# Kernel tuning notes

Measured on AMD Instinct MI355X. Metric: run time of the kernel, lower is better.

## Reference

```python
import jax, jax.numpy as jnp
import numpy as np

DIM, HEADS = 128, 8
DH = DIM // HEADS
SCALE = DH ** -0.5
N, E = 50000, 800000


def setup_inputs() -> dict:
    key = jax.random.key(0)
    ks = jax.random.split(key, 12)
    w = lambda k: jax.random.normal(k, (DIM, DIM), dtype=jnp.float32) * 0.02
    b = lambda k: jax.random.normal(k, (DIM,), dtype=jnp.float32) * 0.02
    return {
        "q_nodes": jax.random.normal(ks[0], (N, DIM), dtype=jnp.float32),
        "k_edges": jax.random.normal(ks[1], (E, DIM), dtype=jnp.float32),
        "v_edges": jax.random.normal(ks[2], (E, DIM), dtype=jnp.float32),
        "edge_index": jax.random.randint(ks[3], (2, E), 0, N, dtype=jnp.int64),
        "Wq": w(ks[4]), "bq": b(ks[5]),
        "Wk": w(ks[6]), "bk": b(ks[7]),
        "Wv": w(ks[8]), "bv": b(ks[9]),
        "Wo": w(ks[10]), "bo": b(ks[11]),
    }


def reference(q_nodes, k_edges, v_edges, edge_index, Wq, bq, Wk, bk, Wv, bv, Wo, bo):
    n, e = q_nodes.shape[0], k_edges.shape[0]
    dst = edge_index[0]  # src (edge_index[1]) is unused by the module
    q = (q_nodes @ Wq.T + bq).reshape(n, HEADS, DH)
    k = (k_edges @ Wk.T + bk).reshape(e, HEADS, DH)
    v = (v_edges @ Wv.T + bv).reshape(e, HEADS, DH)
    # per-edge score: dot(q[dst], k) per head -> [E, H]
    score = jnp.einsum('ehd,ehd->eh', q[dst], k) * SCALE
    # segment (per-dst-node) softmax over edges, numerically stable
    m = jax.ops.segment_max(score, dst, num_segments=n)          # [N, H]
    ex = jnp.exp(score - m[dst])                                  # [E, H]
    s = jax.ops.segment_sum(ex, dst, num_segments=n)             # [N, H]
    w = ex / (s[dst] + 1e-16)                                     # [E, H]
    weighted_v = (v * w[..., None]).reshape(e, DIM)               # [E, dim]
    aggr = jax.ops.segment_sum(weighted_v, dst, num_segments=n)  # [N, dim]
    return aggr @ Wo.T + bo
```

## Files before the change

### kernel.cpp

```cpp
#include <hip/hip_runtime.h>

#define TM 64
#define NTHREADS 256
#define PAD 132

typedef __attribute__((ext_vector_type(8))) short short8;
typedef __attribute__((ext_vector_type(4))) float f32x4;

__device__ __forceinline__ short f2bf(float f) {
  union { float f; unsigned u; } uf; uf.f = f;
  unsigned r = uf.u + 0x7FFFu + ((uf.u >> 16) & 1u);
  return (short)(r >> 16);
}
__device__ __forceinline__ float bf2f(short s) {
  union { unsigned u; float f; } uf; uf.u = ((unsigned)(unsigned short)s) << 16;
  return uf.f;
}
__device__ __forceinline__ short8 pack8(float4 a, float4 b) {
  short8 r;
  r[0] = f2bf(a.x); r[1] = f2bf(a.y); r[2] = f2bf(a.z); r[3] = f2bf(a.w);
  r[4] = f2bf(b.x); r[5] = f2bf(b.y); r[6] = f2bf(b.z); r[7] = f2bf(b.w);
  return r;
}


__global__ __launch_bounds__(512) void proj_mfma(
    const float* __restrict__ X, const short* __restrict__ Wb,
    const float* __restrict__ bias, float* __restrict__ Y, int M, float scale) {
  __shared__ short Xb[8192];
  int t = threadIdx.x;
  int w = t >> 6, l = t & 63, g = l >> 4, c = l & 15;
  short8 wf[4];
#pragma unroll
  for (int kc = 0; kc < 4; ++kc)
    wf[kc] = *(const short8*)(Wb + (w * 16 + c) * 128 + kc * 32 + g * 8);
  float4 b4 = *(const float4*)(bias + w * 16 + g * 4);

  for (int rb = blockIdx.x * 64; rb < M; rb += gridDim.x * 64) {
    {
      int r = t >> 3, q8 = t & 7;
      int row = rb + r; if (row >= M) row = M - 1;
      const float4* xs = (const float4*)(X + (size_t)row * 128 + q8 * 16);
      float4 x0 = xs[0], x1 = xs[1], x2 = xs[2], x3 = xs[3];
      int sw = (r & 7) << 4;
      *(short8*)((char*)Xb + r * 256 + ((q8 * 32) ^ sw)) = pack8(x0, x1);
      *(short8*)((char*)Xb + r * 256 + ((q8 * 32 + 16) ^ sw)) = pack8(x2, x3);
    }
    __syncthreads();
#pragma unroll
    for (int et = 0; et < 4; ++et) {
      int rl = et * 16 + c;
      f32x4 acc = {};
      int sw = (rl & 7) << 4;
#pragma unroll
      for (int kc = 0; kc < 4; ++kc) {
        short8 xb = *(const short8*)((char*)Xb + rl * 256 + ((kc * 64 + g * 16) ^ sw));
        acc = __builtin_amdgcn_mfma_f32_16x16x32_bf16(wf[kc], xb, acc, 0, 0, 0);
      }
      int row = rb + rl;
      if (row < M) {
        float4 o;
        o.x = (acc[0] + b4.x) * scale; o.y = (acc[1] + b4.y) * scale;
        o.z = (acc[2] + b4.z) * scale; o.w = (acc[3] + b4.w) * scale;
        *(float4*)(Y + (size_t)row * 128 + w * 16 + g * 4) = o;
      }
    }
    __syncthreads();
  }
}


__global__ __launch_bounds__(512) void proj_mfma_h(
    const float* __restrict__ X, const short* __restrict__ Wb,
    const float* __restrict__ bias, short* __restrict__ Yh, int M, float scale) {
  __shared__ short Xb[8192];
  int t = threadIdx.x;
  int w = t >> 6, l = t & 63, g = l >> 4, c = l & 15;
  short8 wf[4];
#pragma unroll
  for (int kc = 0; kc < 4; ++kc)
    wf[kc] = *(const short8*)(Wb + (w * 16 + c) * 128 + kc * 32 + g * 8);
  float4 b4 = *(const float4*)(bias + w * 16 + g * 4);

  for (int rb = blockIdx.x * 64; rb < M; rb += gridDim.x * 64) {
    {
      int r = t >> 3, q8 = t & 7;
      int row = rb + r; if (row >= M) row = M - 1;
      const float4* xs = (const float4*)(X + (size_t)row * 128 + q8 * 16);
      float4 x0 = xs[0], x1 = xs[1], x2 = xs[2], x3 = xs[3];
      int sw = (r & 7) << 4;
      *(short8*)((char*)Xb + r * 256 + ((q8 * 32) ^ sw)) = pack8(x0, x1);
      *(short8*)((char*)Xb + r * 256 + ((q8 * 32 + 16) ^ sw)) = pack8(x2, x3);
    }
    __syncthreads();
#pragma unroll
    for (int et = 0; et < 4; ++et) {
      int rl = et * 16 + c;
      f32x4 acc = {};
      int sw = (rl & 7) << 4;
#pragma unroll
      for (int kc = 0; kc < 4; ++kc) {
        short8 xb = *(const short8*)((char*)Xb + rl * 256 + ((kc * 64 + g * 16) ^ sw));
        acc = __builtin_amdgcn_mfma_f32_16x16x32_bf16(wf[kc], xb, acc, 0, 0, 0);
      }
      int row = rb + rl;
      if (row < M) {
        short4 o;
        o.x = f2bf((acc[0] + b4.x) * scale); o.y = f2bf((acc[1] + b4.y) * scale);
        o.z = f2bf((acc[2] + b4.z) * scale); o.w = f2bf((acc[3] + b4.w) * scale);
        *(short4*)(Yh + (size_t)row * 128 + w * 16 + g * 4) = o;
      }
    }
    __syncthreads();
  }
}


__global__ __launch_bounds__(256) void hist_kernel(const int* __restrict__ dst,
                                                   int* __restrict__ cnt, int E) {
  int e = blockIdx.x * 256 + threadIdx.x;
  if (e < E) atomicAdd(&cnt[dst[e]], 1);
// ... 8 lines not shown
  for (int d = 1; d < 64; d <<= 1) v += __shfl_xor(v, d);
  if ((t & 63) == 0) ws[t >> 6] = v;
  __syncthreads();
  if (t < 16) {
    int x = ws[t];
#pragma unroll
    for (int d = 1; d < 16; d <<= 1) x += __shfl_xor(x, d);
    if (t == 0) part[blockIdx.x] = x;
  }
}

__global__ __launch_bounds__(64) void scan_offs(int* __restrict__ part, int P) {
  int t = threadIdx.x;
  int carry = 0;
  for (int base = 0; base < P; base += 64) {
    int i = base + t;
    int v = (i < P) ? part[i] : 0;
    int x = v;
#pragma unroll
    for (int d = 1; d < 64; d <<= 1) { int y = __shfl_up(x, d); if (t >= d) x += y; }
    if (i < P) part[i] = x - v + carry;
    carry += __shfl(x, 63);
  }
}

__global__ __launch_bounds__(1024) void scan_final(const int* __restrict__ cnt,
                                                   const int* __restrict__ part,
                                                   int* __restrict__ rp,
                                                   int* __restrict__ cur, int N) {
  __shared__ int ws[16];
  __shared__ int wofs[16];
  int t = threadIdx.x, i = blockIdx.x * 1024 + t;
  int lane = t & 63, wid = t >> 6;
  int v = (i < N) ? cnt[i] : 0;
  int x = v;
#pragma unroll
  for (int d = 1; d < 64; d <<= 1) { int y = __shfl_up(x, d); if (lane >= d) x += y; }
  if (lane == 63) ws[wid] = x;
  __syncthreads();
  if (t == 0) {
    int s = 0;
#pragma unroll
    for (int k2 = 0; k2 < 16; ++k2) { int tmp = ws[k2]; wofs[k2] = s; s += tmp; }
  }
  __syncthreads();
  int incl = x + wofs[wid] + part[blockIdx.x];
  int excl = incl - v;
  if (i < N) {
    rp[i] = excl; cur[i] = excl;
    if (i == N - 1) rp[N] = incl;
  }
}

__global__ __launch_bounds__(256) void perm_kernel(const int* __restrict__ dst,
                                                   int* __restrict__ cursor,
                                                   int* __restrict__ perm, int E) {
  int e = blockIdx.x * 256 + threadIdx.x;
  if (e < E) perm[e] = atomicAdd(&cursor[dst[e]], 1);
}

__global__ __launch_bounds__(256) void wprep4(
    const float* __restrict__ Wq, const float* __restrict__ Wk,
    const float* __restrict__ Wv, const float* __restrict__ Wo,
    short* __restrict__ wqb, short* __restrict__ wkb,
    short* __restrict__ wvb, short* __restrict__ wob) {
  int i = blockIdx.x * 256 + threadIdx.x;
  if (i < 16384) {
    wqb[i] = f2bf(Wq[i]); wkb[i] = f2bf(Wk[i]);
    wvb[i] = f2bf(Wv[i]); wob[i] = f2bf(Wo[i]);
  }
}


__global__ __launch_bounds__(512) void edge_mfma7(
    const float* __restrict__ K, const float* __restrict__ V,
    const int* __restrict__ eidx, const int* __restrict__ perm,
    const short* __restrict__ wkb, const short* __restrict__ wvb,
    const float* __restrict__ bk, const short* __restrict__ qpb,
    float* __restrict__ exb, short* __restrict__ wv, int E) {
  __shared__ short Kb[8192];
  __shared__ short Vb[8192];
  __shared__ float exs[512];
  __shared__ int sh_perm[64];
  int t = threadIdx.x;
  int w = t >> 6, l = t & 63, g = l >> 4, c = l & 15;
  float4 bk4 = *(const float4*)(bk + w * 16 + g * 4);
  const short* wkp = wkb + (w * 16 + c) * 128 + g * 8;
  const short* wvp = wvb + (w * 16 + c) * 128 + g * 8;
  const short* qpp = qpb + (size_t)(w * 16 + g * 4);

  int r = t >> 3, q8 = t & 7;
  int sw_st = (r & 7) << 4;
  int b0 = r * 256 + ((q8 * 32) ^ sw_st);
  int stride = gridDim.x * 64;
  int eb = blockIdx.x * 64;

  float4 k0, k1, k2, k3;
  short4 qvb[4];
  int prm_r;
  {
    int row0 = eb + r; if (row0 >= E) row0 = E - 1;
    const float4* ks = (const float4*)(K + (size_t)row0 * 128 + q8 * 16);
    k0 = ks[0]; k1 = ks[1]; k2 = ks[2]; k3 = ks[3];
    prm_r = perm[row0];
#pragma unroll
    for (int et = 0; et < 4; ++et) {
      int e = eb + et * 16 + c; if (e >= E) e = E - 1;
      qvb[et] = *(const short4*)(qpp + (size_t)eidx[e] * 128);
    }
  }

  for (; eb < E; eb += stride) {
    int ebn = eb + stride;
    bool hn = ebn < E;

    __syncthreads();
    *(short8*)((char*)Kb + b0) = pack8(k0, k1);
    *(short8*)((char*)Kb + (b0 ^ 16)) = pack8(k2, k3);
    if (q8 == 0) sh_perm[r] = prm_r;
    short8 wK[4];
#pragma unroll
    for (int kc = 0; kc < 4; ++kc)
      wK[kc] = *(const short8*)(wkp + kc * 32);
    float4 v0, v1, v2, v3;
    {
      int rowv = eb + r; if (rowv >= E) rowv = E - 1;
      const float4* vs = (const float4*)(V + (size_t)rowv * 128 + q8 * 16);
      v0 = vs[0]; v1 = vs[1]; v2 = vs[2]; v3 = vs[3];
    }
    __syncthreads();

    float ex[4];
#pragma unroll
    for (int et = 0; et < 4; ++et) {
      int eloc = et * 16 + c;
      int swr = (eloc & 7) << 4;
      f32x4 acc = {};
#pragma unroll
      for (int kc = 0; kc < 4; ++kc) {
        short8 xb = *(const short8*)((char*)Kb + eloc * 256 + ((kc * 64 + g * 16) ^ swr));
        acc = __builtin_amdgcn_mfma_f32_16x16x32_bf16(wK[kc], xb, acc, 0, 0, 0);
      }
      float s = (acc[0] + bk4.x) * bf2f(qvb[et].x) + (acc[1] + bk4.y) * bf2f(qvb[et].y) +
                (acc[2] + bk4.z) * bf2f(qvb[et].z) + (acc[3] + bk4.w) * bf2f(qvb[et].w);
      s += __shfl_xor(s, 16);
      s += __shfl_xor(s, 32);
      ex[et] = __expf(s);
      if (g == 0) exs[eloc * 8 + w] = ex[et];
    }

    *(short8*)((char*)Vb + b0) = pack8(v0, v1);
    *(short8*)((char*)Vb + (b0 ^ 16)) = pack8(v2, v3);
    short8 wV[4];
#pragma unroll
    for (int kc = 0; kc < 4; ++kc)
      wV[kc] = *(const short8*)(wvp + kc * 32);
    int prm_rn = 0;
    if (hn) {
      int rowk = ebn + r; if (rowk >= E) rowk = E - 1;
      const float4* ks = (const float4*)(K + (size_t)rowk * 128 + q8 * 16);
      k0 = ks[0]; k1 = ks[1]; k2 = ks[2]; k3 = ks[3];
      prm_rn = perm[rowk];
#pragma unroll
      for (int et = 0; et < 4; ++et) {
        int e = ebn + et * 16 + c; if (e >= E) e = E - 1;
        qvb[et] = *(const short4*)(qpp + (size_t)eidx[e] * 128);
      }
    }
    __syncthreads();

#pragma unroll
    for (int et = 0; et < 4; ++et) {
      int eloc = et * 16 + c;
      int swr = (eloc & 7) << 4;
      f32x4 acc = {};
#pragma unroll
      for (int kc = 0; kc < 4; ++kc) {
        short8 xb = *(const short8*)((char*)Vb + eloc * 256 + ((kc * 64 + g * 16) ^ swr));
        acc = __builtin_amdgcn_mfma_f32_16x16x32_bf16(wV[kc], xb, acc, 0, 0, 0);
      }
      short4 sv;
      sv.x = f2bf(acc[0] * ex[et]); sv.y = f2bf(acc[1] * ex[et]);
      sv.z = f2bf(acc[2] * ex[et]); sv.w = f2bf(acc[3] * ex[et]);
      *(short4*)((char*)Kb + eloc * 256 + ((w * 32 + g * 8) ^ swr)) = sv;
    }
    prm_r = prm_rn;
    __syncthreads();

    {
      int row = eb + r;
      if (row < E) {
        int slot = sh_perm[r];
        short8 a = *(const short8*)((char*)Kb + r * 256 + ((q8 * 32) ^ sw_st));
        short8 b = *(const short8*)((char*)Kb + r * 256 + ((q8 * 32 + 16) ^ sw_st));
        *(short8*)(wv + (size_t)slot * 128 + q8 * 16) = a;
        *(short8*)(wv + (size_t)slot * 128 + q8 * 16 + 8) = b;
      }
      if (t < 128) {
        int r2 = t >> 1, half = t & 1;
        if (eb + r2 < E) {
          int slot2 = sh_perm[r2];
          *(float4*)(exb + (size_t)slot2 * 8 + half * 4) =
              *(const float4*)(&exs[r2 * 8 + half * 4]);
        }
      }
    }
  }
}


__global__ __launch_bounds__(256) void pull3(
    const short* __restrict__ wv, const float* __restrict__ exb,
    const int* __restrict__ rp, const float* __restrict__ bv,
    float* __restrict__ aggr, int N) {
  int w = threadIdx.x >> 6, l = threadIdx.x & 63;
  int n = blockIdx.x * 4 + w;
  if (n >= N) return;
  int beg = rp[n], end = rp[n + 1];
  int h = l >> 3;
  float a0 = 0.f, a1 = 0.f, s = 0.f;
  int j = beg;
  for (; j + 1 < end; j += 2) {
    unsigned u0 = *(const unsigned*)(wv + (size_t)j * 128 + l * 2);
    unsigned u1 = *(const unsigned*)(wv + (size_t)(j + 1) * 128 + l * 2);
    float s0 = exb[(size_t)j * 8 + h], s1 = exb[(size_t)(j + 1) * 8 + h];
    a0 += bf2f((short)(u0 & 0xFFFFu)) + bf2f((short)(u1 & 0xFFFFu));
    a1 += bf2f((short)(u0 >> 16)) + bf2f((short)(u1 >> 16));
    s += s0 + s1;
  }
  if (j < end) {
    unsigned u0 = *(const unsigned*)(wv + (size_t)j * 128 + l * 2);
    s += exb[(size_t)j * 8 + h];
    a0 += bf2f((short)(u0 & 0xFFFFu));
    a1 += bf2f((short)(u0 >> 16));
  }
  float2 o;
  if (end > beg) {
    float inv = 1.f / (s + 1e-16f);
    float2 bvv = *(const float2*)(bv + l * 2);
    o.x = a0 * inv + bvv.x; o.y = a1 * inv + bvv.y;
  } else {
    o.x = 0.f; o.y = 0.f;
  }
  *(float2*)(aggr + (size_t)n * 128 + l * 2) = o;
}


__device__ __forceinline__ void stage_x(float (*Xs)[PAD], const float* __restrict__ X,
                                        int rowbase, int M, int t) {
#pragma unroll
  for (int i = 0; i < 8; ++i) {
    int idx = t + NTHREADS * i;
    int r = idx >> 5, q = idx & 31;
    int row = rowbase + r;
    if (row >= M) row = M - 1;
    const float4 v = *(const float4*)(X + (size_t)row * 128 + q * 4);
    *(float4*)(&Xs[r][q * 4]) = v;
  }
}

__device__ __forceinline__ void gemm_tile(const float (*Xs)[PAD], float (*WT)[PAD],
                                          const float* __restrict__ W,
                                          float acc[8][4], int r0, int c0, int t) {
#pragma unroll 1
  for (int kk = 0; kk < 128; kk += 32) {
    {
      int j = t >> 1, half = t & 1;
      const float* src = W + j * 128 + kk + half * 16;
      float4 a = *(const float4*)(src);
      float4 b = *(const float4*)(src + 4);
      float4 c = *(const float4*)(src + 8);
      float4 d = *(const float4*)(src + 12);
      int cb = half * 16;
      WT[cb + 0][j] = a.x;  WT[cb + 1][j] = a.y;  WT[cb + 2][j] = a.z;  WT[cb + 3][j] = a.w;
      WT[cb + 4][j] = b.x;  WT[cb + 5][j] = b.y;  WT[cb + 6][j] = b.z;  WT[cb + 7][j] = b.w;
      WT[cb + 8][j] = c.x;  WT[cb + 9][j] = c.y;  WT[cb + 10][j] = c.z; WT[cb + 11][j] = c.w;
      WT[cb + 12][j] = d.x; WT[cb + 13][j] = d.y; WT[cb + 14][j] = d.z; WT[cb + 15][j] = d.w;
    }
    __syncthreads();
#pragma unroll
    for (int c2 = 0; c2 < 16; ++c2) {
      float4 wa = *(const float4*)(&WT[2 * c2][c0]);
      float4 wb = *(const float4*)(&WT[2 * c2 + 1][c0]);
#pragma unroll
      for (int i = 0; i < 8; ++i) {
        float2 xv = *(const float2*)(&Xs[r0 + i][kk + 2 * c2]);
        acc[i][0] = fmaf(xv.x, wa.x, acc[i][0]);
        acc[i][1] = fmaf(xv.x, wa.y, acc[i][1]);
        acc[i][2] = fmaf(xv.x, wa.z, acc[i][2]);
        acc[i][3] = fmaf(xv.x, wa.w, acc[i][3]);
        acc[i][0] = fmaf(xv.y, wb.x, acc[i][0]);
        acc[i][1] = fmaf(xv.y, wb.y, acc[i][1]);
        acc[i][2] = fmaf(xv.y, wb.z, acc[i][2]);
        acc[i][3] = fmaf(xv.y, wb.w, acc[i][3]);
      }
    }
    __syncthreads();
// ... 95 lines not shown
  int B0 = blockIdx.x * TM;
#pragma unroll
  for (int i = 0; i < 8; ++i) {
    int idx = t + NTHREADS * i;
    int r = idx >> 5, q = idx & 31;
    int row = B0 + r;
    if (row >= M) row = M - 1;
    float4 v = *(const float4*)(aggr + (size_t)row * 128 + q * 4);
    float inv = 1.0f / (s_sum[(size_t)row * 8 + (q >> 2)] + 1e-16f);
    v.x *= inv; v.y *= inv; v.z *= inv; v.w *= inv;
    *(float4*)(&Xs[r][q * 4]) = v;
  }
  __syncthreads();
  int r0 = (t >> 5) * 8, m = t & 31, c0 = m * 4;
  float acc[8][4] = {};
  gemm_tile(Xs, WT, W, acc, r0, c0, t);
  float4 bv = ((const float4*)b)[m];
#pragma unroll
  for (int i = 0; i < 8; ++i) {
    int row = B0 + r0 + i;
    if (row < M) {
      float4 o;
      o.x = acc[i][0] + bv.x; o.y = acc[i][1] + bv.y;
      o.z = acc[i][2] + bv.z; o.w = acc[i][3] + bv.w;
      *(float4*)(Y + (size_t)row * 128 + c0) = o;
    }
  }
}


extern "C" void kernel_launch(void* const* d_in, const int* in_sizes, int n_in,
                              void* d_out, int out_size, void* d_ws, size_t ws_size,
                              hipStream_t stream) {
  const float* q_nodes = (const float*)d_in[0];
  const float* k_edges = (const float*)d_in[1];
  const float* v_edges = (const float*)d_in[2];
  const int* eidx = (const int*)d_in[3];
  const float* Wq = (const float*)d_in[4];
  const float* bq = (const float*)d_in[5];
  const float* Wk = (const float*)d_in[6];
  const float* bk = (const float*)d_in[7];
  const float* Wv = (const float*)d_in[8];
  const float* bv = (const float*)d_in[9];
  const float* Wo = (const float*)d_in[10];
  const float* bo = (const float*)d_in[11];

  int N = in_sizes[0] / 128;
  int E = in_sizes[1] / 128;
  int P = (N + 1023) / 1024;

  size_t off = 0;
  auto alloc = [&](size_t b) { size_t o = off; off += (b + 255) & ~(size_t)255; return o; };
  size_t o_qpb  = alloc((size_t)N * 128 * 2);
  size_t o_aggr = alloc((size_t)N * 128 * 4);
  size_t o_exb  = alloc((size_t)E * 8 * 4);
  size_t o_rp   = alloc(((size_t)N + 1) * 4);
  size_t o_cur  = alloc((size_t)N * 4);
  size_t o_cnt  = alloc((size_t)N * 4);
  size_t o_perm = alloc((size_t)E * 4);
  size_t o_part = alloc((size_t)(P + 1) * 4);
  size_t o_wqb  = alloc((size_t)16384 * 2);
  size_t o_wkb  = alloc((size_t)16384 * 2);
  size_t o_wvb  = alloc((size_t)16384 * 2);
  size_t o_wob  = alloc((size_t)16384 * 2);
  size_t o_wv   = alloc((size_t)E * 128 * 2);

  if (off <= ws_size) {
    char* base = (char*)d_ws;
    short* qpb   = (short*)(base + o_qpb);
    float* aggr  = (float*)(base + o_aggr);
    float* exb   = (float*)(base + o_exb);
    int*   rp    = (int*)(base + o_rp);
    int*   cur   = (int*)(base + o_cur);
    int*   cnt   = (int*)(base + o_cnt);
    int*   perm  = (int*)(base + o_perm);
    int*   part  = (int*)(base + o_part);
    short* wqb   = (short*)(base + o_wqb);
    short* wkb   = (short*)(base + o_wkb);
    short* wvb   = (short*)(base + o_wvb);
    short* wob   = (short*)(base + o_wob);
    short* wvbuf = (short*)(base + o_wv);

    hipMemsetAsync(cnt, 0, (size_t)N * 4, stream);
    wprep4<<<64, 256, 0, stream>>>(Wq, Wk, Wv, Wo, wqb, wkb, wvb, wob);
    proj_mfma_h<<<(N + 63) / 64, 512, 0, stream>>>(q_nodes, wqb, bq, qpb, N, 0.25f);
    hist_kernel<<<(E + 255) / 256, 256, 0, stream>>>(eidx, cnt, E);
    scan_part<<<P, 1024, 0, stream>>>(cnt, part, N);
    scan_offs<<<1, 64, 0, stream>>>(part, P);
    scan_final<<<P, 1024, 0, stream>>>(cnt, part, rp, cur, N);
    perm_kernel<<<(E + 255) / 256, 256, 0, stream>>>(eidx, cur, perm, E);

    int eblk = (E + 63) / 64; if (eblk > 1024) eblk = 1024;
    edge_mfma7<<<eblk, 512, 0, stream>>>(k_edges, v_edges, eidx, perm, wkb, wvb,
                                         bk, qpb, exb, wvbuf, E);
    pull3<<<(N + 3) / 4, 256, 0, stream>>>(wvbuf, exb, rp, bv, aggr, N);
    proj_mfma<<<(N + 63) / 64, 512, 0, stream>>>(aggr, wob, bo, (float*)d_out, N, 1.0f);
  } else {
    float* q_proj = (float*)d_ws;
    float* s_sum  = q_proj + (size_t)N * 128;
    float* aggr   = s_sum + (size_t)N * 8;
    hipMemsetAsync(s_sum, 0, (size_t)N * 136 * sizeof(float), stream);
    int nblk = (N + TM - 1) / TM;
    int eblk = (E + TM - 1) / TM;
    proj_kernel<<<nblk, NTHREADS, 0, stream>>>(q_nodes, Wq, bq, q_proj, N);
    edge_kernel<<<eblk, NTHREADS, 0, stream>>>(k_edges, v_edges, eidx, Wk, bk, Wv, bv,
                                               q_proj, s_sum, aggr, E);
    out_kernel<<<nblk, NTHREADS, 0, stream>>>(aggr, s_sum, Wo, bo, (float*)d_out, N);
  }
}
```

Baseline: 420.0 us.

## Defer V projection until after aggregation via per-head raw-V sums

The V projection moves out of the per-edge kernel and is applied after aggregation, using linearity. Each node gathers raw fp32 V rows by sorted edge id and accumulates eight per-head weighted sums, stored as bf16 [N,8,128]. A fused kernel then applies Wv per head block plus bias, and Wo plus bias, in one pass. This removes the per-edge V MFMA and the E x 128 bf16 weighted-V buffer, at the cost of random fp32 V gathers, an 8x wider per-node intermediate and an extra eid scatter.

```diff
diff --git a/kernel.cpp b/kernel.cpp
--- a/kernel.cpp
+++ b/kernel.cpp
@@ -21,52 +21,6 @@
   r[0] = f2bf(a.x); r[1] = f2bf(a.y); r[2] = f2bf(a.z); r[3] = f2bf(a.w);
   r[4] = f2bf(b.x); r[5] = f2bf(b.y); r[6] = f2bf(b.z); r[7] = f2bf(b.w);
   return r;
-}
-
-
-__global__ __launch_bounds__(512) void proj_mfma(
-    const float* __restrict__ X, const short* __restrict__ Wb,
-    const float* __restrict__ bias, float* __restrict__ Y, int M, float scale) {
-  __shared__ short Xb[8192];
-  int t = threadIdx.x;
-  int w = t >> 6, l = t & 63, g = l >> 4, c = l & 15;
-  short8 wf[4];
-#pragma unroll
-  for (int kc = 0; kc < 4; ++kc)
-    wf[kc] = *(const short8*)(Wb + (w * 16 + c) * 128 + kc * 32 + g * 8);
-  float4 b4 = *(const float4*)(bias + w * 16 + g * 4);
-
-  for (int rb = blockIdx.x * 64; rb < M; rb += gridDim.x * 64) {
-    {
-      int r = t >> 3, q8 = t & 7;
-      int row = rb + r; if (row >= M) row = M - 1;
-      const float4* xs = (const float4*)(X + (size_t)row * 128 + q8 * 16);
-      float4 x0 = xs[0], x1 = xs[1], x2 = xs[2], x3 = xs[3];
-      int sw = (r & 7) << 4;
-      *(short8*)((char*)Xb + r * 256 + ((q8 * 32) ^ sw)) = pack8(x0, x1);
-      *(short8*)((char*)Xb + r * 256 + ((q8 * 32 + 16) ^ sw)) = pack8(x2, x3);
-    }
-    __syncthreads();
-#pragma unroll
-    for (int et = 0; et < 4; ++et) {
-      int rl = et * 16 + c;
-      f32x4 acc = {};
-      int sw = (rl & 7) << 4;
-#pragma unroll
-      for (int kc = 0; kc < 4; ++kc) {
-        short8 xb = *(const short8*)((char*)Xb + rl * 256 + ((kc * 64 + g * 16) ^ sw));
-        acc = __builtin_amdgcn_mfma_f32_16x16x32_bf16(wf[kc], xb, acc, 0, 0, 0);
-      }
-      int row = rb + rl;
-      if (row < M) {
-        float4 o;
-        o.x = (acc[0] + b4.x) * scale; o.y = (acc[1] + b4.y) * scale;
-        o.z = (acc[2] + b4.z) * scale; o.w = (acc[3] + b4.w) * scale;
-        *(float4*)(Y + (size_t)row * 128 + w * 16 + g * 4) = o;
-      }
-    }
-    __syncthreads();
-  }
 }
 
 
@@ -181,11 +135,15 @@
   }
 }
 
-__global__ __launch_bounds__(256) void perm_kernel(const int* __restrict__ dst,
-                                                   int* __restrict__ cursor,
-                                                   int* __restrict__ perm, int E) {
+__global__ __launch_bounds__(256) void perm_eid(const int* __restrict__ dst,
+                                                int* __restrict__ cursor,
+                                                int* __restrict__ perm,
+                                                int* __restrict__ eid, int E) {
   int e = blockIdx.x * 256 + threadIdx.x;
-  if (e < E) perm[e] = atomicAdd(&cursor[dst[e]], 1);
+  if (e < E) {
+    int p = atomicAdd(&cursor[dst[e]], 1);
+    perm[e] = p; eid[p] = e;
+  }
 }
 
 __global__ __launch_bounds__(256) void wprep4(
@@ -201,40 +159,33 @@
 }
 
 
-__global__ __launch_bounds__(512) void edge_mfma7(
-    const float* __restrict__ K, const float* __restrict__ V,
-    const int* __restrict__ eidx, const int* __restrict__ perm,
-    const short* __restrict__ wkb, const short* __restrict__ wvb,
+__global__ __launch_bounds__(512) void kproj_score(
+    const float* __restrict__ K, const int* __restrict__ eidx,
+    const int* __restrict__ perm, const short* __restrict__ wkb,
     const float* __restrict__ bk, const short* __restrict__ qpb,
-    float* __restrict__ exb, short* __restrict__ wv, int E) {
+    float* __restrict__ exb, int E) {
   __shared__ short Kb[8192];
-  __shared__ short Vb[8192];
-  __shared__ float exs[512];
-  __shared__ int sh_perm[64];
   int t = threadIdx.x;
   int w = t >> 6, l = t & 63, g = l >> 4, c = l & 15;
   float4 bk4 = *(const float4*)(bk + w * 16 + g * 4);
   const short* wkp = wkb + (w * 16 + c) * 128 + g * 8;
-  const short* wvp = wvb + (w * 16 + c) * 128 + g * 8;
   const short* qpp = qpb + (size_t)(w * 16 + g * 4);
-
   int r = t >> 3, q8 = t & 7;
-  int sw_st = (r & 7) << 4;
-  int b0 = r * 256 + ((q8 * 32) ^ sw_st);
+  int b0 = r * 256 + ((q8 * 32) ^ ((r & 7) << 4));
   int stride = gridDim.x * 64;
   int eb = blockIdx.x * 64;
 
   float4 k0, k1, k2, k3;
   short4 qvb[4];
-  int prm_r;
+  int p[4];
   {
     int row0 = eb + r; if (row0 >= E) row0 = E - 1;
     const float4* ks = (const float4*)(K + (size_t)row0 * 128 + q8 * 16);
     k0 = ks[0]; k1 = ks[1]; k2 = ks[2]; k3 = ks[3];
-    prm_r = perm[row0];
 #pragma unroll
     for (int et = 0; et < 4; ++et) {
       int e = eb + et * 16 + c; if (e >= E) e = E - 1;
+      p[et] = perm[e];
       qvb[et] = *(const short4*)(qpp + (size_t)eidx[e] * 128);
     }
   }
@@ -242,24 +193,15 @@
   for (; eb < E; eb += stride) {
     int ebn = eb + stride;
     bool hn = ebn < E;
-
     __syncthreads();
     *(short8*)((char*)Kb + b0) = pack8(k0, k1);
     *(short8*)((char*)Kb + (b0 ^ 16)) = pack8(k2, k3);
-    if (q8 == 0) sh_perm[r] = prm_r;
     short8 wK[4];
 #pragma unroll
     for (int kc = 0; kc < 4; ++kc)
       wK[kc] = *(const short8*)(wkp + kc * 32);
-    float4 v0, v1, v2, v3;
-    {
-      int rowv = eb + r; if (rowv >= E) rowv = E - 1;
-      const float4* vs = (const float4*)(V + (size_t)rowv * 128 + q8 * 16);
-      v0 = vs[0]; v1 = vs[1]; v2 = vs[2]; v3 = vs[3];
-    }
-    __syncthreads();
-
-    float ex[4];
+    __syncthreads();
+
 #pragma unroll
     for (int et = 0; et < 4; ++et) {
       int eloc = et * 16 + c;
@@ -274,104 +216,126 @@
                 (acc[2] + bk4.z) * bf2f(qvb[et].z) + (acc[3] + bk4.w) * bf2f(qvb[et].w);
       s += __shfl_xor(s, 16);
       s += __shfl_xor(s, 32);
-      ex[et] = __expf(s);
-      if (g == 0) exs[eloc * 8 + w] = ex[et];
-    }
-
-    *(short8*)((char*)Vb + b0) = pack8(v0, v1);
-    *(short8*)((char*)Vb + (b0 ^ 16)) = pack8(v2, v3);
-    short8 wV[4];
-#pragma unroll
-    for (int kc = 0; kc < 4; ++kc)
-      wV[kc] = *(const short8*)(wvp + kc * 32);
-    int prm_rn = 0;
+      if (g == 0) exb[(size_t)p[et] * 8 + w] = __expf(s);
+    }
+
     if (hn) {
       int rowk = ebn + r; if (rowk >= E) rowk = E - 1;
       const float4* ks = (const float4*)(K + (size_t)rowk * 128 + q8 * 16);
       k0 = ks[0]; k1 = ks[1]; k2 = ks[2]; k3 = ks[3];
-      prm_rn = perm[rowk];
 #pragma unroll
       for (int et = 0; et < 4; ++et) {
         int e = ebn + et * 16 + c; if (e >= E) e = E - 1;
+        p[et] = perm[e];
         qvb[et] = *(const short4*)(qpp + (size_t)eidx[e] * 128);
       }
     }
-    __syncthreads();
-
-#pragma unroll
-    for (int et = 0; et < 4; ++et) {
-      int eloc = et * 16 + c;
-      int swr = (eloc & 7) << 4;
-      f32x4 acc = {};
-#pragma unroll
-      for (int kc = 0; kc < 4; ++kc) {
-        short8 xb = *(const short8*)((char*)Vb + eloc * 256 + ((kc * 64 + g * 16) ^ swr));
-        acc = __builtin_amdgcn_mfma_f32_16x16x32_bf16(wV[kc], xb, acc, 0, 0, 0);
-      }
-      short4 sv;
-      sv.x = f2bf(acc[0] * ex[et]); sv.y = f2bf(acc[1] * ex[et]);
-      sv.z = f2bf(acc[2] * ex[et]); sv.w = f2bf(acc[3] * ex[et]);
-      *(short4*)((char*)Kb + eloc * 256 + ((w * 32 + g * 8) ^ swr)) = sv;
-    }
-    prm_r = prm_rn;
-    __syncthreads();
-
-    {
-      int row = eb + r;
-      if (row < E) {
-        int slot = sh_perm[r];
-        short8 a = *(const short8*)((char*)Kb + r * 256 + ((q8 * 32) ^ sw_st));
-        short8 b = *(const short8*)((char*)Kb + r * 256 + ((q8 * 32 + 16) ^ sw_st));
-        *(short8*)(wv + (size_t)slot * 128 + q8 * 16) = a;
-        *(short8*)(wv + (size_t)slot * 128 + q8 * 16 + 8) = b;
-      }
-      if (t < 128) {
-        int r2 = t >> 1, half = t & 1;
-        if (eb + r2 < E) {
-          int slot2 = sh_perm[r2];
-          *(float4*)(exb + (size_t)slot2 * 8 + half * 4) =
-              *(const float4*)(&exs[r2 * 8 + half * 4]);
-        }
-      }
-    }
-  }
-}
-
-
-__global__ __launch_bounds__(256) void pull3(
-    const short* __restrict__ wv, const float* __restrict__ exb,
-    const int* __restrict__ rp, const float* __restrict__ bv,
-    float* __restrict__ aggr, int N) {
-  int w = threadIdx.x >> 6, l = threadIdx.x & 63;
-  int n = blockIdx.x * 4 + w;
+  }
+}
+
+
+__global__ __launch_bounds__(256) void vpull(
+    const float* __restrict__ V, const int* __restrict__ eid,
+    const int* __restrict__ rp, const float* __restrict__ exb,
+    short* __restrict__ araw, int N) {
+  int wn = threadIdx.x >> 6, l = threadIdx.x & 63;
+  int n = blockIdx.x * 4 + wn;
   if (n >= N) return;
   int beg = rp[n], end = rp[n + 1];
-  int h = l >> 3;
-  float a0 = 0.f, a1 = 0.f, s = 0.f;
-  int j = beg;
-  for (; j + 1 < end; j += 2) {
-    unsigned u0 = *(const unsigned*)(wv + (size_t)j * 128 + l * 2);
-    unsigned u1 = *(const unsigned*)(wv + (size_t)(j + 1) * 128 + l * 2);
-    float s0 = exb[(size_t)j * 8 + h], s1 = exb[(size_t)(j + 1) * 8 + h];
-    a0 += bf2f((short)(u0 & 0xFFFFu)) + bf2f((short)(u1 & 0xFFFFu));
-    a1 += bf2f((short)(u0 >> 16)) + bf2f((short)(u1 >> 16));
-    s += s0 + s1;
-  }
-  if (j < end) {
-    unsigned u0 = *(const unsigned*)(wv + (size_t)j * 128 + l * 2);
-    s += exb[(size_t)j * 8 + h];
-    a0 += bf2f((short)(u0 & 0xFFFFu));
-    a1 += bf2f((short)(u0 >> 16));
-  }
-  float2 o;
-  if (end > beg) {
-    float inv = 1.f / (s + 1e-16f);
-    float2 bvv = *(const float2*)(bv + l * 2);
-    o.x = a0 * inv + bvv.x; o.y = a1 * inv + bvv.y;
-  } else {
-    o.x = 0.f; o.y = 0.f;
-  }
-  *(float2*)(aggr + (size_t)n * 128 + l * 2) = o;
+  float a[8][2] = {};
+  float ssum[8] = {};
+  if (beg < end) {
+    int e = eid[beg];
+    float2 v = *(const float2*)(V + (size_t)e * 128 + l * 2);
+    float4 x0 = *(const float4*)(exb + (size_t)beg * 8);
+    float4 x1 = *(const float4*)(exb + (size_t)beg * 8 + 4);
+    for (int j = beg; j < end; ++j) {
+      int jn = (j + 1 < end) ? j + 1 : j;
+      int en = eid[jn];
+      float2 vn = *(const float2*)(V + (size_t)en * 128 + l * 2);
+      float4 y0 = *(const float4*)(exb + (size_t)jn * 8);
+      float4 y1 = *(const float4*)(exb + (size_t)jn * 8 + 4);
+      a[0][0] = fmaf(x0.x, v.x, a[0][0]); a[0][1] = fmaf(x0.x, v.y, a[0][1]);
+      a[1][0] = fmaf(x0.y, v.x, a[1][0]); a[1][1] = fmaf(x0.y, v.y, a[1][1]);
+      a[2][0] = fmaf(x0.z, v.x, a[2][0]); a[2][1] = fmaf(x0.z, v.y, a[2][1]);
+      a[3][0] = fmaf(x0.w, v.x, a[3][0]); a[3][1] = fmaf(x0.w, v.y, a[3][1]);
+      a[4][0] = fmaf(x1.x, v.x, a[4][0]); a[4][1] = fmaf(x1.x, v.y, a[4][1]);
+      a[5][0] = fmaf(x1.y, v.x, a[5][0]); a[5][1] = fmaf(x1.y, v.y, a[5][1]);
+      a[6][0] = fmaf(x1.z, v.x, a[6][0]); a[6][1] = fmaf(x1.z, v.y, a[6][1]);
+      a[7][0] = fmaf(x1.w, v.x, a[7][0]); a[7][1] = fmaf(x1.w, v.y, a[7][1]);
+      ssum[0] += x0.x; ssum[1] += x0.y; ssum[2] += x0.z; ssum[3] += x0.w;
+      ssum[4] += x1.x; ssum[5] += x1.y; ssum[6] += x1.z; ssum[7] += x1.w;
+      v = vn; x0 = y0; x1 = y1;
+    }
+  }
+  short* base = araw + (size_t)n * 1024 + l * 2;
+#pragma unroll
+  for (int h = 0; h < 8; ++h) {
+    float inv = 1.f / (ssum[h] + 1e-16f);
+    unsigned pk = ((unsigned)(unsigned short)f2bf(a[h][1] * inv) << 16) |
+                  (unsigned short)f2bf(a[h][0] * inv);
+    *(unsigned*)(base + h * 128) = pk;
+  }
+}
+
+
+__global__ __launch_bounds__(512) void vproj_out(
+    const short* __restrict__ araw, const int* __restrict__ cnt,
+    const float* __restrict__ bvv, const short* __restrict__ wvb,
+    const short* __restrict__ wob, const float* __restrict__ bo,
+    float* __restrict__ Y, int N) {
+  __shared__ short Xb[8192];
+  int t = threadIdx.x;
+  int w = t >> 6, l = t & 63, g = l >> 4, c = l & 15;
+  float4 bv4 = *(const float4*)(bvv + w * 16 + g * 4);
+  float4 bo4 = *(const float4*)(bo + w * 16 + g * 4);
+  short8 wvf[4], wof[4];
+#pragma unroll
+  for (int kc = 0; kc < 4; ++kc) {
+    wvf[kc] = *(const short8*)(wvb + (w * 16 + c) * 128 + kc * 32 + g * 8);
+    wof[kc] = *(const short8*)(wob + (w * 16 + c) * 128 + kc * 32 + g * 8);
+  }
+
+  for (int rb = blockIdx.x * 64; rb < N; rb += gridDim.x * 64) {
+#pragma unroll
+    for (int et = 0; et < 4; ++et) {
+      int rl = et * 16 + c;
+      int row = rb + rl; int rowc = row < N ? row : N - 1;
+      const short* ap = araw + (size_t)rowc * 1024 + w * 128 + g * 8;
+      f32x4 acc = {};
+#pragma unroll
+      for (int kc = 0; kc < 4; ++kc) {
+        short8 xb = *(const short8*)(ap + kc * 32);
+        acc = __builtin_amdgcn_mfma_f32_16x16x32_bf16(wvf[kc], xb, acc, 0, 0, 0);
+      }
+      float m = (cnt[rowc] > 0) ? 1.f : 0.f;
+      short4 sv;
+      sv.x = f2bf(acc[0] + bv4.x * m); sv.y = f2bf(acc[1] + bv4.y * m);
+      sv.z = f2bf(acc[2] + bv4.z * m); sv.w = f2bf(acc[3] + bv4.w * m);
+      *(short4*)((char*)Xb + rl * 256 + ((w * 32 + g * 8) ^ ((rl & 7) << 4))) = sv;
+    }
+    __syncthreads();
+
+#pragma unroll
+    for (int et = 0; et < 4; ++et) {
+      int rl = et * 16 + c;
+      f32x4 acc = {};
+      int sw = (rl & 7) << 4;
+#pragma unroll
+      for (int kc = 0; kc < 4; ++kc) {
+        short8 xb = *(const short8*)((char*)Xb + rl * 256 + ((kc * 64 + g * 16) ^ sw));
+        acc = __builtin_amdgcn_mfma_f32_16x16x32_bf16(wof[kc], xb, acc, 0, 0, 0);
+      }
+      int row = rb + rl;
+      if (row < N) {
+        float4 o;
+        o.x = acc[0] + bo4.x; o.y = acc[1] + bo4.y;
+        o.z = acc[2] + bo4.z; o.w = acc[3] + bo4.w;
+        *(float4*)(Y + (size_t)row * 128 + w * 16 + g * 4) = o;
+      }
+    }
+    __syncthreads();
+  }
 }
 
 
@@ -573,34 +537,34 @@
   size_t off = 0;
   auto alloc = [&](size_t b) { size_t o = off; off += (b + 255) & ~(size_t)255; return o; };
   size_t o_qpb  = alloc((size_t)N * 128 * 2);
-  size_t o_aggr = alloc((size_t)N * 128 * 4);
+  size_t o_araw = alloc((size_t)N * 1024 * 2);
   size_t o_exb  = alloc((size_t)E * 8 * 4);
   size_t o_rp   = alloc(((size_t)N + 1) * 4);
   size_t o_cur  = alloc((size_t)N * 4);
   size_t o_cnt  = alloc((size_t)N * 4);
   size_t o_perm = alloc((size_t)E * 4);
+  size_t o_eid  = alloc((size_t)E * 4);
   size_t o_part = alloc((size_t)(P + 1) * 4);
   size_t o_wqb  = alloc((size_t)16384 * 2);
   size_t o_wkb  = alloc((size_t)16384 * 2);
   size_t o_wvb  = alloc((size_t)16384 * 2);
   size_t o_wob  = alloc((size_t)16384 * 2);
-  size_t o_wv   = alloc((size_t)E * 128 * 2);
 
   if (off <= ws_size) {
     char* base = (char*)d_ws;
-    short* qpb   = (short*)(base + o_qpb);
-    float* aggr  = (float*)(base + o_aggr);
-    float* exb   = (float*)(base + o_exb);
-    int*   rp    = (int*)(base + o_rp);
-    int*   cur   = (int*)(base + o_cur);
-    int*   cnt   = (int*)(base + o_cnt);
-    int*   perm  = (int*)(base + o_perm);
-    int*   part  = (int*)(base + o_part);
-    short* wqb   = (short*)(base + o_wqb);
-    short* wkb   = (short*)(base + o_wkb);
-    short* wvb   = (short*)(base + o_wvb);
-    short* wob   = (short*)(base + o_wob);
-    short* wvbuf = (short*)(base + o_wv);
+    short* qpb  = (short*)(base + o_qpb);
+    short* araw = (short*)(base + o_araw);
+    float* exb  = (float*)(base + o_exb);
+    int*   rp   = (int*)(base + o_rp);
+    int*   cur  = (int*)(base + o_cur);
+    int*   cnt  = (int*)(base + o_cnt);
+    int*   perm = (int*)(base + o_perm);
+    int*   eid  = (int*)(base + o_eid);
+    int*   part = (int*)(base + o_part);
+    short* wqb  = (short*)(base + o_wqb);
+    short* wkb  = (short*)(base + o_wkb);
+    short* wvb  = (short*)(base + o_wvb);
+    short* wob  = (short*)(base + o_wob);
 
     hipMemsetAsync(cnt, 0, (size_t)N * 4, stream);
     wprep4<<<64, 256, 0, stream>>>(Wq, Wk, Wv, Wo, wqb, wkb, wvb, wob);
@@ -609,13 +573,13 @@
     scan_part<<<P, 1024, 0, stream>>>(cnt, part, N);
     scan_offs<<<1, 64, 0, stream>>>(part, P);
     scan_final<<<P, 1024, 0, stream>>>(cnt, part, rp, cur, N);
-    perm_kernel<<<(E + 255) / 256, 256, 0, stream>>>(eidx, cur, perm, E);
+    perm_eid<<<(E + 255) / 256, 256, 0, stream>>>(eidx, cur, perm, eid, E);
 
     int eblk = (E + 63) / 64; if (eblk > 1024) eblk = 1024;
-    edge_mfma7<<<eblk, 512, 0, stream>>>(k_edges, v_edges, eidx, perm, wkb, wvb,
-                                         bk, qpb, exb, wvbuf, E);
-    pull3<<<(N + 3) / 4, 256, 0, stream>>>(wvbuf, exb, rp, bv, aggr, N);
-    proj_mfma<<<(N + 63) / 64, 512, 0, stream>>>(aggr, wob, bo, (float*)d_out, N, 1.0f);
+    kproj_score<<<eblk, 512, 0, stream>>>(k_edges, eidx, perm, wkb, bk, qpb, exb, E);
+    vpull<<<(N + 3) / 4, 256, 0, stream>>>(v_edges, eid, rp, exb, araw, N);
+    vproj_out<<<(N + 63) / 64, 512, 0, stream>>>(araw, cnt, bv, wvb, wob, bo,
+                                                 (float*)d_out, N);
   } else {
     float* q_proj = (float*)d_ws;
     float* s_sum  = q_proj + (size_t)N * 128;
```

Result: slower. 456.2 us (+8.6%).

## Prefetch K and V together and scatter edge outputs directly to global

Applied to the files above, without the earlier changes.

The edge kernel now loads both K and V for the next tile one iteration ahead and stages both into shared memory before a single barrier. It also writes the weighted V fragments and exp scores straight from MFMA registers to their permuted global slots, instead of staging them in shared memory first. This removes two barriers and the shared-memory restaging pass per tile, aiming for better latency hiding. The trade-off is higher register pressure and smaller, less coalesced scattered global stores.

```diff
diff --git a/kernel.cpp b/kernel.cpp
--- a/kernel.cpp
+++ b/kernel.cpp
@@ -201,7 +201,7 @@
 }
 
 
-__global__ __launch_bounds__(512) void edge_mfma7(
+__global__ __launch_bounds__(512) void edge_mfma9(
     const float* __restrict__ K, const float* __restrict__ V,
     const int* __restrict__ eidx, const int* __restrict__ perm,
     const short* __restrict__ wkb, const short* __restrict__ wvb,
@@ -209,7 +209,6 @@
     float* __restrict__ exb, short* __restrict__ wv, int E) {
   __shared__ short Kb[8192];
   __shared__ short Vb[8192];
-  __shared__ float exs[512];
   __shared__ int sh_perm[64];
   int t = threadIdx.x;
   int w = t >> 6, l = t & 63, g = l >> 4, c = l & 15;
@@ -219,18 +218,19 @@
   const short* qpp = qpb + (size_t)(w * 16 + g * 4);
 
   int r = t >> 3, q8 = t & 7;
-  int sw_st = (r & 7) << 4;
-  int b0 = r * 256 + ((q8 * 32) ^ sw_st);
+  int b0 = r * 256 + ((q8 * 32) ^ ((r & 7) << 4));
   int stride = gridDim.x * 64;
   int eb = blockIdx.x * 64;
 
-  float4 k0, k1, k2, k3;
+  float4 k0, k1, k2, k3, v0, v1, v2, v3;
   short4 qvb[4];
   int prm_r;
   {
     int row0 = eb + r; if (row0 >= E) row0 = E - 1;
     const float4* ks = (const float4*)(K + (size_t)row0 * 128 + q8 * 16);
     k0 = ks[0]; k1 = ks[1]; k2 = ks[2]; k3 = ks[3];
+    const float4* vs = (const float4*)(V + (size_t)row0 * 128 + q8 * 16);
+    v0 = vs[0]; v1 = vs[1]; v2 = vs[2]; v3 = vs[3];
     prm_r = perm[row0];
 #pragma unroll
     for (int et = 0; et < 4; ++et) {
@@ -246,24 +246,39 @@
     __syncthreads();
     *(short8*)((char*)Kb + b0) = pack8(k0, k1);
     *(short8*)((char*)Kb + (b0 ^ 16)) = pack8(k2, k3);
+    *(short8*)((char*)Vb + b0) = pack8(v0, v1);
+    *(short8*)((char*)Vb + (b0 ^ 16)) = pack8(v2, v3);
     if (q8 == 0) sh_perm[r] = prm_r;
+    __syncthreads();
+
     short8 wK[4];
 #pragma unroll
     for (int kc = 0; kc < 4; ++kc)
       wK[kc] = *(const short8*)(wkp + kc * 32);
-    float4 v0, v1, v2, v3;
-    {
-      int rowv = eb + r; if (rowv >= E) rowv = E - 1;
-      const float4* vs = (const float4*)(V + (size_t)rowv * 128 + q8 * 16);
+
+    short4 qvn[4];
+    int prm_rn = 0;
+    if (hn) {
+      int rowk = ebn + r; if (rowk >= E) rowk = E - 1;
+      const float4* ks = (const float4*)(K + (size_t)rowk * 128 + q8 * 16);
+      k0 = ks[0]; k1 = ks[1]; k2 = ks[2]; k3 = ks[3];
+      const float4* vs = (const float4*)(V + (size_t)rowk * 128 + q8 * 16);
       v0 = vs[0]; v1 = vs[1]; v2 = vs[2]; v3 = vs[3];
-    }
-    __syncthreads();
+      prm_rn = perm[rowk];
+#pragma unroll
+      for (int et = 0; et < 4; ++et) {
+        int e = ebn + et * 16 + c; if (e >= E) e = E - 1;
+        qvn[et] = *(const short4*)(qpp + (size_t)eidx[e] * 128);
+      }
+    }
 
     float ex[4];
+    int sl[4];
 #pragma unroll
     for (int et = 0; et < 4; ++et) {
       int eloc = et * 16 + c;
       int swr = (eloc & 7) << 4;
+      sl[et] = sh_perm[eloc];
       f32x4 acc = {};
 #pragma unroll
       for (int kc = 0; kc < 4; ++kc) {
@@ -275,28 +290,13 @@
       s += __shfl_xor(s, 16);
       s += __shfl_xor(s, 32);
       ex[et] = __expf(s);
-      if (g == 0) exs[eloc * 8 + w] = ex[et];
-    }
-
-    *(short8*)((char*)Vb + b0) = pack8(v0, v1);
-    *(short8*)((char*)Vb + (b0 ^ 16)) = pack8(v2, v3);
+      if (g == 0) exb[(size_t)sl[et] * 8 + w] = ex[et];
+    }
+
     short8 wV[4];
 #pragma unroll
     for (int kc = 0; kc < 4; ++kc)
       wV[kc] = *(const short8*)(wvp + kc * 32);
-    int prm_rn = 0;
-    if (hn) {
-      int rowk = ebn + r; if (rowk >= E) rowk = E - 1;
-      const float4* ks = (const float4*)(K + (size_t)rowk * 128 + q8 * 16);
-      k0 = ks[0]; k1 = ks[1]; k2 = ks[2]; k3 = ks[3];
-      prm_rn = perm[rowk];
-#pragma unroll
-      for (int et = 0; et < 4; ++et) {
-        int e = ebn + et * 16 + c; if (e >= E) e = E - 1;
-        qvb[et] = *(const short4*)(qpp + (size_t)eidx[e] * 128);
-      }
-    }
-    __syncthreads();
 
 #pragma unroll
     for (int et = 0; et < 4; ++et) {
@@ -311,29 +311,12 @@
       short4 sv;
       sv.x = f2bf(acc[0] * ex[et]); sv.y = f2bf(acc[1] * ex[et]);
       sv.z = f2bf(acc[2] * ex[et]); sv.w = f2bf(acc[3] * ex[et]);
-      *(short4*)((char*)Kb + eloc * 256 + ((w * 32 + g * 8) ^ swr)) = sv;
-    }
+      *(short4*)(wv + (size_t)sl[et] * 128 + w * 16 + g * 4) = sv;
+    }
+
+#pragma unroll
+    for (int et = 0; et < 4; ++et) qvb[et] = qvn[et];
     prm_r = prm_rn;
-    __syncthreads();
-
-    {
-      int row = eb + r;
-      if (row < E) {
-        int slot = sh_perm[r];
-        short8 a = *(const short8*)((char*)Kb + r * 256 + ((q8 * 32) ^ sw_st));
-        short8 b = *(const short8*)((char*)Kb + r * 256 + ((q8 * 32 + 16) ^ sw_st));
-        *(short8*)(wv + (size_t)slot * 128 + q8 * 16) = a;
-        *(short8*)(wv + (size_t)slot * 128 + q8 * 16 + 8) = b;
-      }
-      if (t < 128) {
-        int r2 = t >> 1, half = t & 1;
-        if (eb + r2 < E) {
-          int slot2 = sh_perm[r2];
-          *(float4*)(exb + (size_t)slot2 * 8 + half * 4) =
-              *(const float4*)(&exs[r2 * 8 + half * 4]);
-        }
-      }
-    }
   }
 }
 
@@ -612,7 +595,7 @@
     perm_kernel<<<(E + 255) / 256, 256, 0, stream>>>(eidx, cur, perm, E);
 
     int eblk = (E + 63) / 64; if (eblk > 1024) eblk = 1024;
-    edge_mfma7<<<eblk, 512, 0, stream>>>(k_edges, v_edges, eidx, perm, wkb, wvb,
+    edge_mfma9<<<eblk, 512, 0, stream>>>(k_edges, v_edges, eidx, perm, wkb, wvb,
                                          bk, qpb, exb, wvbuf, E);
     pull3<<<(N + 3) / 4, 256, 0, stream>>>(wvbuf, exb, rp, bv, aggr, N);
     proj_mfma<<<(N + 63) / 64, 512, 0, stream>>>(aggr, wob, bo, (float*)d_out, N, 1.0f);
```

New measurement: 442.2 us. +5.3%, slower.

## Restructure edge kernel to 256 threads with two heads per wave over 32-edge tiles

Applied to the files above, without the earlier changes.

The edge projection kernel moves from 512 threads handling 64 edges per tile (one head per wave) to 256 threads handling 32 edges per tile, with each wave computing two heads in sequence. Shared memory per block is halved and the grid cap doubles, so more, smaller blocks can be resident and the per-tile barriers involve fewer waves. In exchange each wave does more serial MFMA work and more register-held weight loads per tile, and tiles are smaller, which may reduce memory-level parallelism per block.

```diff
diff --git a/kernel.cpp b/kernel.cpp
--- a/kernel.cpp
+++ b/kernel.cpp
@@ -201,31 +201,36 @@
 }
 
 
-__global__ __launch_bounds__(512) void edge_mfma7(
+__global__ __launch_bounds__(256) void edge_mfma10(
     const float* __restrict__ K, const float* __restrict__ V,
     const int* __restrict__ eidx, const int* __restrict__ perm,
     const short* __restrict__ wkb, const short* __restrict__ wvb,
     const float* __restrict__ bk, const short* __restrict__ qpb,
     float* __restrict__ exb, short* __restrict__ wv, int E) {
-  __shared__ short Kb[8192];
-  __shared__ short Vb[8192];
-  __shared__ float exs[512];
-  __shared__ int sh_perm[64];
+  __shared__ short Kb[4096];
+  __shared__ short Vb[4096];
+  __shared__ float exs[256];
+  __shared__ int sh_perm[32];
   int t = threadIdx.x;
-  int w = t >> 6, l = t & 63, g = l >> 4, c = l & 15;
-  float4 bk4 = *(const float4*)(bk + w * 16 + g * 4);
-  const short* wkp = wkb + (w * 16 + c) * 128 + g * 8;
-  const short* wvp = wvb + (w * 16 + c) * 128 + g * 8;
-  const short* qpp = qpb + (size_t)(w * 16 + g * 4);
+  int w4 = t >> 6, l = t & 63, g = l >> 4, c = l & 15;
+  int h0 = w4 * 2, h1 = h0 + 1;
+  float4 bk4a = *(const float4*)(bk + h0 * 16 + g * 4);
+  float4 bk4b = *(const float4*)(bk + h1 * 16 + g * 4);
+  const short* wkpa = wkb + (h0 * 16 + c) * 128 + g * 8;
+  const short* wkpb = wkb + (h1 * 16 + c) * 128 + g * 8;
+  const short* wvpa = wvb + (h0 * 16 + c) * 128 + g * 8;
+  const short* wvpb = wvb + (h1 * 16 + c) * 128 + g * 8;
+  const short* qppa = qpb + h0 * 16 + g * 4;
+  const short* qppb = qpb + h1 * 16 + g * 4;
 
   int r = t >> 3, q8 = t & 7;
   int sw_st = (r & 7) << 4;
   int b0 = r * 256 + ((q8 * 32) ^ sw_st);
-  int stride = gridDim.x * 64;
-  int eb = blockIdx.x * 64;
+  int stride = gridDim.x * 32;
+  int eb = blockIdx.x * 32;
 
   float4 k0, k1, k2, k3;
-  short4 qvb[4];
+  short4 qa[2], qb[2];
   int prm_r;
   {
     int row0 = eb + r; if (row0 >= E) row0 = E - 1;
@@ -233,9 +238,11 @@
     k0 = ks[0]; k1 = ks[1]; k2 = ks[2]; k3 = ks[3];
     prm_r = perm[row0];
 #pragma unroll
-    for (int et = 0; et < 4; ++et) {
+    for (int et = 0; et < 2; ++et) {
       int e = eb + et * 16 + c; if (e >= E) e = E - 1;
-      qvb[et] = *(const short4*)(qpp + (size_t)eidx[e] * 128);
+      size_t de = (size_t)eidx[e] * 128;
+      qa[et] = *(const short4*)(qppa + de);
+      qb[et] = *(const short4*)(qppb + de);
     }
   }
 
@@ -247,10 +254,6 @@
     *(short8*)((char*)Kb + b0) = pack8(k0, k1);
     *(short8*)((char*)Kb + (b0 ^ 16)) = pack8(k2, k3);
     if (q8 == 0) sh_perm[r] = prm_r;
-    short8 wK[4];
-#pragma unroll
-    for (int kc = 0; kc < 4; ++kc)
-      wK[kc] = *(const short8*)(wkp + kc * 32);
     float4 v0, v1, v2, v3;
     {
       int rowv = eb + r; if (rowv >= E) rowv = E - 1;
@@ -259,31 +262,56 @@
     }
     __syncthreads();
 
-    float ex[4];
-#pragma unroll
-    for (int et = 0; et < 4; ++et) {
-      int eloc = et * 16 + c;
-      int swr = (eloc & 7) << 4;
-      f32x4 acc = {};
-#pragma unroll
-      for (int kc = 0; kc < 4; ++kc) {
-        short8 xb = *(const short8*)((char*)Kb + eloc * 256 + ((kc * 64 + g * 16) ^ swr));
-        acc = __builtin_amdgcn_mfma_f32_16x16x32_bf16(wK[kc], xb, acc, 0, 0, 0);
-      }
-      float s = (acc[0] + bk4.x) * bf2f(qvb[et].x) + (acc[1] + bk4.y) * bf2f(qvb[et].y) +
-                (acc[2] + bk4.z) * bf2f(qvb[et].z) + (acc[3] + bk4.w) * bf2f(qvb[et].w);
-      s += __shfl_xor(s, 16);
-      s += __shfl_xor(s, 32);
-      ex[et] = __expf(s);
-      if (g == 0) exs[eloc * 8 + w] = ex[et];
+    float exa[2], exB[2];
+    int sl[2];
+    {
+      short8 wK[4];
+#pragma unroll
+      for (int kc = 0; kc < 4; ++kc) wK[kc] = *(const short8*)(wkpa + kc * 32);
+#pragma unroll
+      for (int et = 0; et < 2; ++et) {
+        int eloc = et * 16 + c;
+        int swr = (eloc & 7) << 4;
+        sl[et] = sh_perm[eloc];
+        f32x4 acc = {};
+#pragma unroll
+        for (int kc = 0; kc < 4; ++kc) {
+          short8 xb = *(const short8*)((char*)Kb + eloc * 256 + ((kc * 64 + g * 16) ^ swr));
+          acc = __builtin_amdgcn_mfma_f32_16x16x32_bf16(wK[kc], xb, acc, 0, 0, 0);
+        }
+        float s = (acc[0] + bk4a.x) * bf2f(qa[et].x) + (acc[1] + bk4a.y) * bf2f(qa[et].y) +
+                  (acc[2] + bk4a.z) * bf2f(qa[et].z) + (acc[3] + bk4a.w) * bf2f(qa[et].w);
+        s += __shfl_xor(s, 16);
+        s += __shfl_xor(s, 32);
+        exa[et] = __expf(s);
+        if (g == 0) exs[eloc * 8 + h0] = exa[et];
+      }
+    }
+    {
+      short8 wK[4];
+#pragma unroll
+      for (int kc = 0; kc < 4; ++kc) wK[kc] = *(const short8*)(wkpb + kc * 32);
+#pragma unroll
+      for (int et = 0; et < 2; ++et) {
+        int eloc = et * 16 + c;
+        int swr = (eloc & 7) << 4;
+        f32x4 acc = {};
+#pragma unroll
+        for (int kc = 0; kc < 4; ++kc) {
+          short8 xb = *(const short8*)((char*)Kb + eloc * 256 + ((kc * 64 + g * 16) ^ swr));
+          acc = __builtin_amdgcn_mfma_f32_16x16x32_bf16(wK[kc], xb, acc, 0, 0, 0);
+        }
+        float s = (acc[0] + bk4b.x) * bf2f(qb[et].x) + (acc[1] + bk4b.y) * bf2f(qb[et].y) +
+                  (acc[2] + bk4b.z) * bf2f(qb[et].z) + (acc[3] + bk4b.w) * bf2f(qb[et].w);
+        s += __shfl_xor(s, 16);
+        s += __shfl_xor(s, 32);
+        exB[et] = __expf(s);
+        if (g == 0) exs[eloc * 8 + h1] = exB[et];
+      }
     }
 
     *(short8*)((char*)Vb + b0) = pack8(v0, v1);
     *(short8*)((char*)Vb + (b0 ^ 16)) = pack8(v2, v3);
-    short8 wV[4];
-#pragma unroll
-    for (int kc = 0; kc < 4; ++kc)
-      wV[kc] = *(const short8*)(wvp + kc * 32);
     int prm_rn = 0;
     if (hn) {
       int rowk = ebn + r; if (rowk >= E) rowk = E - 1;
@@ -291,27 +319,54 @@
       k0 = ks[0]; k1 = ks[1]; k2 = ks[2]; k3 = ks[3];
       prm_rn = perm[rowk];
 #pragma unroll
-      for (int et = 0; et < 4; ++et) {
+      for (int et = 0; et < 2; ++et) {
         int e = ebn + et * 16 + c; if (e >= E) e = E - 1;
-        qvb[et] = *(const short4*)(qpp + (size_t)eidx[e] * 128);
-      }
-    }
-    __syncthreads();
-
-#pragma unroll
-    for (int et = 0; et < 4; ++et) {
-      int eloc = et * 16 + c;
-      int swr = (eloc & 7) << 4;
-      f32x4 acc = {};
-#pragma unroll
-      for (int kc = 0; kc < 4; ++kc) {
-        short8 xb = *(const short8*)((char*)Vb + eloc * 256 + ((kc * 64 + g * 16) ^ swr));
-        acc = __builtin_amdgcn_mfma_f32_16x16x32_bf16(wV[kc], xb, acc, 0, 0, 0);
-      }
-      short4 sv;
-      sv.x = f2bf(acc[0] * ex[et]); sv.y = f2bf(acc[1] * ex[et]);
-      sv.z = f2bf(acc[2] * ex[et]); sv.w = f2bf(acc[3] * ex[et]);
-      *(short4*)((char*)Kb + eloc * 256 + ((w * 32 + g * 8) ^ swr)) = sv;
+        size_t de = (size_t)eidx[e] * 128;
+        qa[et] = *(const short4*)(qppa + de);
+        qb[et] = *(const short4*)(qppb + de);
+      }
+    }
+    __syncthreads();
+
+    {
+      short8 wV[4];
+#pragma unroll
+      for (int kc = 0; kc < 4; ++kc) wV[kc] = *(const short8*)(wvpa + kc * 32);
+#pragma unroll
+      for (int et = 0; et < 2; ++et) {
+        int eloc = et * 16 + c;
+        int swr = (eloc & 7) << 4;
+        f32x4 acc = {};
+#pragma unroll
+        for (int kc = 0; kc < 4; ++kc) {
+          short8 xb = *(const short8*)((char*)Vb + eloc * 256 + ((kc * 64 + g * 16) ^ swr));
+          acc = __builtin_amdgcn_mfma_f32_16x16x32_bf16(wV[kc], xb, acc, 0, 0, 0);
+        }
+        short4 sv;
+        sv.x = f2bf(acc[0] * exa[et]); sv.y = f2bf(acc[1] * exa[et]);
+        sv.z = f2bf(acc[2] * exa[et]); sv.w = f2bf(acc[3] * exa[et]);
+        *(short4*)((char*)Kb + eloc * 256 + ((h0 * 32 + g * 8) ^ swr)) = sv;
+      }
+    }
+    {
+      short8 wV[4];
+#pragma unroll
+      for (int kc = 0; kc < 4; ++kc) wV[kc] = *(const short8*)(wvpb + kc * 32);
+#pragma unroll
+      for (int et = 0; et < 2; ++et) {
+        int eloc = et * 16 + c;
+        int swr = (eloc & 7) << 4;
+        f32x4 acc = {};
+#pragma unroll
+        for (int kc = 0; kc < 4; ++kc) {
+          short8 xb = *(const short8*)((char*)Vb + eloc * 256 + ((kc * 64 + g * 16) ^ swr));
+          acc = __builtin_amdgcn_mfma_f32_16x16x32_bf16(wV[kc], xb, acc, 0, 0, 0);
+        }
+        short4 sv;
+        sv.x = f2bf(acc[0] * exB[et]); sv.y = f2bf(acc[1] * exB[et]);
+        sv.z = f2bf(acc[2] * exB[et]); sv.w = f2bf(acc[3] * exB[et]);
+        *(short4*)((char*)Kb + eloc * 256 + ((h1 * 32 + g * 8) ^ swr)) = sv;
+      }
     }
     prm_r = prm_rn;
     __syncthreads();
@@ -325,7 +380,7 @@
         *(short8*)(wv + (size_t)slot * 128 + q8 * 16) = a;
         *(short8*)(wv + (size_t)slot * 128 + q8 * 16 + 8) = b;
       }
-      if (t < 128) {
+      if (t < 64) {
         int r2 = t >> 1, half = t & 1;
         if (eb + r2 < E) {
           int slot2 = sh_perm[r2];
@@ -611,9 +666,9 @@
     scan_final<<<P, 1024, 0, stream>>>(cnt, part, rp, cur, N);
     perm_kernel<<<(E + 255) / 256, 256, 0, stream>>>(eidx, cur, perm, E);
 
-    int eblk = (E + 63) / 64; if (eblk > 1024) eblk = 1024;
-    edge_mfma7<<<eblk, 512, 0, stream>>>(k_edges, v_edges, eidx, perm, wkb, wvb,
-                                         bk, qpb, exb, wvbuf, E);
+    int eblk = (E + 31) / 32; if (eblk > 2048) eblk = 2048;
+    edge_mfma10<<<eblk, 256, 0, stream>>>(k_edges, v_edges, eidx, perm, wkb, wvb,
+                                          bk, qpb, exb, wvbuf, E);
     pull3<<<(N + 3) / 4, 256, 0, stream>>>(wvbuf, exb, rp, bv, aggr, N);
     proj_mfma<<<(N + 63) / 64, 512, 0, stream>>>(aggr, wob, bo, (float*)d_out, N, 1.0f);
   } else {
```

Result: no change. 420.5 us (+0.1%).
